# Optimization experiments

Hardware: AMD Instinct MI355X
Metric: run time of the kernel (lower is better)

The kernel has to match this reference:

```python
import jax, jax.numpy as jnp
import numpy as np
import math

D_MODEL = 1024
NUM_HEADS = 16
D_K = D_MODEL // NUM_HEADS
SEQ = 2048
BATCH = 2


def setup_inputs() -> dict:
    key = jax.random.key(0)
    ks = jax.random.split(key, 11)
    s = 1.0 / math.sqrt(D_MODEL)
    return {
        "query": jax.random.normal(ks[0], (SEQ, BATCH, D_MODEL), jnp.float32),
        "key": jax.random.normal(ks[1], (SEQ, BATCH, D_MODEL), jnp.float32),
        "value": jax.random.normal(ks[2], (SEQ, BATCH, D_MODEL), jnp.float32),
        "Wq": jax.random.normal(ks[3], (D_MODEL, D_MODEL), jnp.float32) * s,
        "bq": jnp.zeros((D_MODEL,), jnp.float32),
        "Wk": jax.random.normal(ks[4], (D_MODEL, D_MODEL), jnp.float32) * s,
        "bk": jnp.zeros((D_MODEL,), jnp.float32),
        "Wv": jax.random.normal(ks[5], (D_MODEL, D_MODEL), jnp.float32) * s,
        "bv": jnp.zeros((D_MODEL,), jnp.float32),
        "Wo": jax.random.normal(ks[6], (D_MODEL, D_MODEL), jnp.float32) * s,
        "bo": jnp.zeros((D_MODEL,), jnp.float32),
    }


def _split_heads(x):
    # [S, B, D] -> [S, B, H, d_k]
    S, B, _ = x.shape
    return x.reshape(S, B, NUM_HEADS, D_K)


def reference(query, key, value, Wq, bq, Wk, bk, Wv, bv, Wo, bo):
    # torch Linear: y = x @ W.T + b
    q = _split_heads(query @ Wq.T + bq)   # [S,B,H,dk]
    k = _split_heads(key @ Wk.T + bk)
    v = _split_heads(value @ Wv.T + bv)
    # score[q,k,b,h] = sum_d q[q,b,h,d] k[k,b,h,d]
    score = jnp.einsum('qbhd,kbhd->qkbh', q, k) / math.sqrt(D_K)
    attn = jax.nn.softmax(score, axis=1)  # Softmax(dim=1) == over key axis
    out = jnp.einsum('qkbh,kbhd->qbhd', attn, v)  # [S,B,H,dk]
    S, B = out.shape[0], out.shape[1]
    out = out.reshape(S, B, NUM_HEADS * D_K)
    return out @ Wo.T + bo
```

## Files before the change

### kernel.cpp

```cpp
#include <hip/hip_runtime.h>

typedef unsigned short u16;
typedef short s16x8 __attribute__((ext_vector_type(8)));
typedef short s16x4 __attribute__((ext_vector_type(4)));
typedef float f32x4 __attribute__((ext_vector_type(4)));

#define MFMA_BF16(A,B,C) __builtin_amdgcn_mfma_f32_16x16x32_bf16(A,B,C,0,0,0)

#if defined(__has_builtin)
#if __has_builtin(__builtin_amdgcn_mfma_f32_16x16x16bf16_1k)
#define HAVE_MFMA16 1
#define MFMA16(A,B,C) __builtin_amdgcn_mfma_f32_16x16x16bf16_1k(A,B,C,0,0,0)
#endif
#endif

static constexpr int DMODEL = 1024;
static constexpr int SEQn   = 2048;
static constexpr int BATCH  = 2;
static constexpr int NH     = 16;
static constexpr int DKn    = 64;
static constexpr int ROWST  = BATCH*DMODEL;
static constexpr float QSCALE = 0.18033688011112042f;

__device__ __forceinline__ u16 f2bf(float f) {
    unsigned u = __builtin_bit_cast(unsigned, f);
    u += 0x7FFFu + ((u >> 16) & 1u);
    return (u16)(u >> 16);
}

#if defined(__has_builtin)
#if __has_builtin(__builtin_amdgcn_cvt_pk_bf16_f32)
#define HAVE_PKBF16 1
#endif
#endif
#ifdef HAVE_PKBF16
typedef __bf16 bf16x2 __attribute__((ext_vector_type(2)));
__device__ __forceinline__ unsigned pk2bf(float a, float b) {
    bf16x2 t = __builtin_amdgcn_cvt_pk_bf16_f32(a, b);
    return __builtin_bit_cast(unsigned, t);
}
#else
__device__ __forceinline__ unsigned pk2bf(float a, float b) {
    return (unsigned)f2bf(a) | ((unsigned)f2bf(b) << 16);
}
#endif

__device__ __forceinline__ void gld_lds16(const u16* g, u16* l) {
    __builtin_amdgcn_global_load_lds(
        (const __attribute__((address_space(1))) void*)g,
        (__attribute__((address_space(3))) void*)l,
        16, 0, 0);
}

__global__ void cvt_bf16(const float* __restrict__ q, const float* __restrict__ k,
                         const float* __restrict__ v, const float* __restrict__ wq,
                         const float* __restrict__ wk, const float* __restrict__ wv,
                         const float* __restrict__ wo,
                         u16* __restrict__ qb, u16* __restrict__ kb, u16* __restrict__ vb,
                         u16* __restrict__ wqb, u16* __restrict__ wkb, u16* __restrict__ wvb,
                         u16* __restrict__ wob)
{
    const int z = blockIdx.z;
    const float* S; u16* D; size_t n;
    switch (z) {
        case 0: S = q;  D = qb;  n = 4194304; break;
        case 1: S = k;  D = kb;  n = 4194304; break;
        case 2: S = v;  D = vb;  n = 4194304; break;
        case 3: S = wq; D = wqb; n = 1048576; break;
        case 4: S = wk; D = wkb; n = 1048576; break;
        case 5: S = wv; D = wvb; n = 1048576; break;
        default: S = wo; D = wob; n = 1048576; break;
    }
    const size_t i = ((size_t)blockIdx.x * 256 + threadIdx.x) * 8;
    if (i >= n) return;
    float4 a = *(const float4*)(S + i);
    float4 b = *(const float4*)(S + i + 4);
    uint4 pk;
    pk.x = pk2bf(a.x, a.y); pk.y = pk2bf(a.z, a.w);
    pk.z = pk2bf(b.x, b.y); pk.w = pk2bf(b.z, b.w);
    *(uint4*)(D + i) = pk;
}

template<bool FINAL>
__global__ __launch_bounds__(256, 2)
void gemm_bt(const u16* __restrict__ A0, const u16* __restrict__ A1, const u16* __restrict__ A2,
             const u16* __restrict__ W0, const u16* __restrict__ W1, const u16* __restrict__ W2,
             const float* __restrict__ B0, const float* __restrict__ B1, const float* __restrict__ B2,
             void* __restrict__ O0, void* __restrict__ O1, void* __restrict__ O2)
{
    const u16* A; const u16* W; const float* bias; void* Outv;
    const int z = blockIdx.z;
    if (z == 0)      { A = A0; W = W0; bias = B0; Outv = O0; }
    else if (z == 1) { A = A1; W = W1; bias = B1; Outv = O1; }
    else             { A = A2; W = W2; bias = B2; Outv = O2; }

    __shared__ alignas(16) u16 SH[FINAL ? 128*128 : 129*128];
    u16* As = SH;
    u16* Bs = SH + 128*64;

    const int tid  = threadIdx.x;
    const int wave = tid >> 6, lane = tid & 63;
    const int quad = lane >> 4, col = lane & 15;
    const int wm = wave & 1, wn = wave >> 1;
    const int m0 = blockIdx.y * 128, n0 = blockIdx.x * 128;

    f32x4 acc[4][4];
#pragma unroll
    for (int i = 0; i < 4; ++i)
#pragma unroll
        for (int j = 0; j < 4; ++j) acc[i][j] = f32x4{0.f,0.f,0.f,0.f};

    for (int kt = 0; kt < DMODEL/64; ++kt) {
        if (kt) __syncthreads();
        const int k0 = kt*64;
#pragma unroll
        for (int i = 0; i < 4; ++i) {
            const int chunk = (i*4 + wave)*64 + lane;
            const int row = chunk >> 3;
            const int kk = ((chunk & 7) ^ (row & 7)) * 8;
            gld_lds16(A + (size_t)(m0 + row)*DMODEL + (k0 + kk), &As[(i*4 + wave)*512]);
            gld_lds16(W + (size_t)(n0 + row)*DMODEL + (k0 + kk), &Bs[(i*4 + wave)*512]);
        }
        __syncthreads();
#pragma unroll
        for (int ks = 0; ks < 2; ++ks) {
            s16x8 af[4], bfr[4];
#pragma unroll
            for (int t = 0; t < 4; ++t) {
                const int ra = wm*64 + t*16 + col;
                af[t]  = *(const s16x8*)&As[ra*64 + (((ks*4 + quad) ^ (ra & 7))*8)];
                const int rb = wn*64 + t*16 + col;
                bfr[t] = *(const s16x8*)&Bs[rb*64 + (((ks*4 + quad) ^ (rb & 7))*8)];
            }
#pragma unroll
            for (int i = 0; i < 4; ++i)
#pragma unroll
                for (int j = 0; j < 4; ++j)
                    acc[i][j] = MFMA_BF16(af[i], bfr[j], acc[i][j]);
        }
    }

    float bv[4];
#pragma unroll
    for (int j = 0; j < 4; ++j) bv[j] = bias[n0 + wn*64 + j*16 + col];

    if (FINAL) {
#pragma unroll
        for (int i = 0; i < 4; ++i)
#pragma unroll
            for (int j = 0; j < 4; ++j) {
                const int n = n0 + wn*64 + j*16 + col;
#pragma unroll
                for (int r = 0; r < 4; ++r) {
                    const int m = m0 + wm*64 + i*16 + quad*4 + r;
                    ((float*)Outv)[(size_t)m*DMODEL + n] = acc[i][j][r] + bv[j];
                }
            }
    } else {
        const float osc = (z == 0) ? QSCALE : 1.f;
        const int SST = (z == 2) ? 129 : 128;
        __syncthreads();
#pragma unroll
        for (int i = 0; i < 4; ++i)
#pragma unroll
            for (int j = 0; j < 4; ++j) {
                const int nl = wn*64 + j*16 + col;
#pragma unroll
                for (int r = 0; r < 4; ++r) {
                    const int ml = wm*64 + i*16 + quad*4 + r;
                    SH[ml*SST + nl] = f2bf((acc[i][j][r] + bv[j])*osc);
                }
            }
        __syncthreads();
        u16* Out = (u16*)Outv;
        if (z < 2) {
#pragma unroll
            for (int t = 0; t < 8; ++t) {
                const int c = t*256 + tid;
                const int ml = c >> 4, n8 = (c & 15)*8;
                uint4 x = *(const uint4*)&SH[ml*128 + n8];
                *(uint4*)(Out + (size_t)(m0 + ml)*DMODEL + n0 + n8) = x;
            }
        } else {
            const int s0 = m0 >> 1;
#pragma unroll
            for (int t = 0; t < 8; ++t) {
                const int c = t*256 + tid;
                const int sc = c & 7;
                const int nl = (c >> 3) & 127;
                const int bb = c >> 10;
                u16 e[8];
#pragma unroll
                for (int j = 0; j < 8; ++j)
                    e[j] = SH[((sc*8 + j)*2 + bb)*129 + nl];
                uint4 x; __builtin_memcpy(&x, e, 16);
                const int ng = n0 + nl, hh = ng >> 6, dd = ng & 63;
                *(uint4*)(Out + (((size_t)bb*NH + hh)*DKn + dd)*SEQn + s0 + sc*8) = x;
            }
        }
    }
}

__global__ __launch_bounds__(256, 2)
void attn_fwd(const u16* __restrict__ Q, const u16* __restrict__ K,
              const u16* __restrict__ Vt, u16* __restrict__ O)
{
    __shared__ alignas(16) u16 Ks[128*64];
    __shared__ alignas(16) u16 Vs[64*128];

    const int qt = blockIdx.x, bh = blockIdx.y;
    const int b = bh >> 4, h = bh & 15;
    const int tid = threadIdx.x;
    const int wave = tid >> 6, lane = tid & 63;
    const int quad = lane >> 4, col = lane & 15;

    const u16* Qh = Q + b*DMODEL + h*DKn;
    const u16* Kh = K + b*DMODEL + h*DKn;
    const u16* Vh = Vt + (size_t)bh*DKn*SEQn;

    const int q0 = qt*128 + wave*32;
    s16x8 qf[2][2];
#pragma unroll
    for (int qg = 0; qg < 2; ++qg)
#pragma unroll
        for (int ks = 0; ks < 2; ++ks)
            qf[qg][ks] = *(const s16x8*)(Qh + (size_t)(q0 + qg*16 + col)*ROWST + ks*32 + quad*8);

    f32x4 o[2][4];
    float dsum[2] = {0.f, 0.f};
#pragma unroll
    for (int qg = 0; qg < 2; ++qg)
#pragma unroll
        for (int dt = 0; dt < 4; ++dt) o[qg][dt] = f32x4{0.f,0.f,0.f,0.f};

    for (int kt = 0; kt < SEQn/128; ++kt) {
        __syncthreads();
#pragma unroll
        for (int i = 0; i < 4; ++i) {
            {
                const int chunk = (i*4 + wave)*64 + lane;
                const int row = chunk >> 3;
                const int kk = ((chunk & 7) ^ (row & 7))*8;
                gld_lds16(Kh + (size_t)(kt*128 + row)*ROWST + kk, &Ks[(i*4 + wave)*512]);
            }
            {
                const int chunk = (i*4 + wave)*64 + lane;
                const int d = chunk >> 4;
                const int kk = ((chunk & 15) ^ (d & 15))*8;
                gld_lds16(Vh + (size_t)d*SEQn + kt*128 + kk, &Vs[(i*4 + wave)*512]);
            }
        }
        __syncthreads();

        f32x4 sfr[2][8];
#pragma unroll
        for (int qg = 0; qg < 2; ++qg)
#pragma unroll
            for (int nt = 0; nt < 8; ++nt) sfr[qg][nt] = f32x4{0.f,0.f,0.f,0.f};
#pragma unroll
        for (int ks = 0; ks < 2; ++ks) {
#pragma unroll
            for (int nt = 0; nt < 8; ++nt) {
                const int key = nt*16 + col;
                const s16x8 kf = *(const s16x8*)&Ks[key*64 + (((ks*4 + quad) ^ (key & 7))*8)];
                sfr[0][nt] = MFMA_BF16(kf, qf[0][ks], sfr[0][nt]);
                sfr[1][nt] = MFMA_BF16(kf, qf[1][ks], sfr[1][nt]);
            }
        }

        s16x4 pk[2][8];
#pragma unroll
        for (int qg = 0; qg < 2; ++qg)
#pragma unroll
            for (int nt = 0; nt < 8; ++nt) {
                float p0 = __builtin_amdgcn_exp2f(sfr[qg][nt][0]);
                float p1 = __builtin_amdgcn_exp2f(sfr[qg][nt][1]);
                float p2 = __builtin_amdgcn_exp2f(sfr[qg][nt][2]);
                float p3 = __builtin_amdgcn_exp2f(sfr[qg][nt][3]);
                dsum[qg] += (p0 + p1) + (p2 + p3);
                unsigned w[2] = { pk2bf(p0, p1), pk2bf(p2, p3) };
                __builtin_memcpy(&pk[qg][nt], w, 8);
            }

#ifdef HAVE_MFMA16
#pragma unroll
        for (int c = 0; c < 8; ++c) {
#pragma unroll
            for (int dt = 0; dt < 4; ++dt) {
                const int d = dt*16 + col;
                const s16x4 vfr = *(const s16x4*)&Vs[d*128 + (((c*2 + (quad>>1)) ^ (d & 15))*8) + (quad & 1)*4];
                o[0][dt] = MFMA16(vfr, pk[0][c], o[0][dt]);
                o[1][dt] = MFMA16(vfr, pk[1][c], o[1][dt]);
            }
        }
#else
        const int a0 = (32*(quad & 1) + col)*4;
#pragma unroll
        for (int qg = 0; qg < 2; ++qg) {
#pragma unroll
            for (int ksp = 0; ksp < 4; ++ksp) {
                int pA[2], pB[2];
                __builtin_memcpy(pA, &pk[qg][ksp*2], 8);
                __builtin_memcpy(pB, &pk[qg][ksp*2 + 1], 8);
                int w[4];
#pragma unroll
                for (int hh = 0; hh < 2; ++hh) {
                    const int ad = a0 + hh*64;
                    const int xA0 = __builtin_amdgcn_ds_bpermute(ad, pA[0]);
                    const int xA1 = __builtin_amdgcn_ds_bpermute(ad, pA[1]);
                    const int xB0 = __builtin_amdgcn_ds_bpermute(ad, pB[0]);
                    const int xB1 = __builtin_amdgcn_ds_bpermute(ad, pB[1]);
                    w[hh*2]     = (quad >= 2) ? xB0 : xA0;
                    w[hh*2 + 1] = (quad >= 2) ? xB1 : xA1;
                }
                s16x8 pfr; __builtin_memcpy(&pfr, w, 16);
#pragma unroll
                for (int dt = 0; dt < 4; ++dt) {
                    const int d = dt*16 + col;
                    const s16x8 vfr = *(const s16x8*)&Vs[d*128 + (((ksp*4 + quad) ^ (d & 15))*8)];
                    o[qg][dt] = MFMA_BF16(vfr, pfr, o[qg][dt]);
                }
            }
        }
#endif
    }

    float inv[2];
#pragma unroll
    for (int qg = 0; qg < 2; ++qg) {
        float d = dsum[qg];
        d += __shfl_xor(d, 16, 64);
        d += __shfl_xor(d, 32, 64);
        inv[qg] = 1.f / d;
    }

#pragma unroll
    for (int qg = 0; qg < 2; ++qg) {
        const int srow = q0 + qg*16 + col;
#pragma unroll
        for (int dt = 0; dt < 4; ++dt) {
            uint2 pko;
            pko.x = pk2bf(o[qg][dt][0]*inv[qg], o[qg][dt][1]*inv[qg]);
            pko.y = pk2bf(o[qg][dt][2]*inv[qg], o[qg][dt][3]*inv[qg]);
            *(uint2*)(O + ((size_t)srow*BATCH + b)*DMODEL + h*DKn + dt*16 + quad*4) = pko;
        }
    }
}

extern "C" void kernel_launch(void* const* d_in, const int* in_sizes, int n_in,
                              void* d_out, int out_size, void* d_ws, size_t ws_size,
                              hipStream_t stream)
{
    const float* q  = (const float*)d_in[0];
    const float* k  = (const float*)d_in[1];
    const float* v  = (const float*)d_in[2];
    const float* Wq = (const float*)d_in[3];
    const float* bq = (const float*)d_in[4];
    const float* Wk = (const float*)d_in[5];
    const float* bk = (const float*)d_in[6];
    const float* Wv = (const float*)d_in[7];
    const float* bv = (const float*)d_in[8];
    const float* Wo = (const float*)d_in[9];
    const float* bo = (const float*)d_in[10];
    float* out = (float*)d_out;

    const size_t N = (size_t)SEQn * BATCH * DMODEL;
    const size_t NW = (size_t)DMODEL * DMODEL;
    u16* qb  = (u16*)d_ws;
    u16* kb  = qb + N;
    u16* vb  = kb + N;
    u16* wqb = vb + N;
    u16* wkb = wqb + NW;
    u16* wvb = wkb + NW;
    u16* wob = wvb + NW;
    u16* Qw  = wob + NW;
    u16* Kw  = Qw + N;
    u16* Vtw = Kw + N;
    u16* AO  = qb;

    cvt_bf16<<<dim3(2048, 1, 7), 256, 0, stream>>>(q, k, v, Wq, Wk, Wv, Wo,
                                                   qb, kb, vb, wqb, wkb, wvb, wob);
    gemm_bt<false><<<dim3(8, 32, 3), 256, 0, stream>>>(qb, kb, vb, wqb, wkb, wvb,
                                                       bq, bk, bv, Qw, Kw, Vtw);
    attn_fwd<<<dim3(16, 32), 256, 0, stream>>>(Qw, Kw, Vtw, AO);
    gemm_bt<true><<<dim3(8, 32, 1), 256, 0, stream>>>(AO, AO, AO, wob, wob, wob,
                                                      bo, bo, bo, out, out, out);
}
```

Baseline: 234.6 us.

## Split attention key tiles across waves with cross-wave LDS reduction of outputs

Each block now handles 32 queries instead of 128. The four waves split each 128-key tile among themselves, with 32 keys per wave, instead of each wave owning separate query rows. Partial outputs and denominators are combined across waves through LDS at the end, and the grid grows fourfold with launch bounds raised to 4 blocks per SM. This aims to increase parallelism and occupancy, but every block now reloads the full K and V tiles for only 32 queries, quadrupling K/V traffic, and adds an LDS reduction step.

```diff
diff --git a/kernel.cpp b/kernel.cpp
--- a/kernel.cpp
+++ b/kernel.cpp
@@ -201,12 +201,13 @@
     }
 }
 
-__global__ __launch_bounds__(256, 2)
+__global__ __launch_bounds__(256, 4)
 void attn_fwd(const u16* __restrict__ Q, const u16* __restrict__ K,
               const u16* __restrict__ Vt, u16* __restrict__ O)
 {
-    __shared__ alignas(16) u16 Ks[128*64];
-    __shared__ alignas(16) u16 Vs[64*128];
+    __shared__ alignas(16) u16 SH[16896];
+    u16* Ks = SH;
+    u16* Vs = SH + 128*64;
 
     const int qt = blockIdx.x, bh = blockIdx.y;
     const int b = bh >> 4, h = bh & 15;
@@ -218,33 +219,32 @@
     const u16* Kh = K + b*DMODEL + h*DKn;
     const u16* Vh = Vt + (size_t)bh*DKn*SEQn;
 
-    const int q0 = qt*128 + wave*32;
+    const int q0 = qt*32;
     s16x8 qf[2][2];
 #pragma unroll
-    for (int qg = 0; qg < 2; ++qg)
+    for (int qb = 0; qb < 2; ++qb)
 #pragma unroll
         for (int ks = 0; ks < 2; ++ks)
-            qf[qg][ks] = *(const s16x8*)(Qh + (size_t)(q0 + qg*16 + col)*ROWST + ks*32 + quad*8);
+            qf[qb][ks] = *(const s16x8*)(Qh + (size_t)(q0 + qb*16 + col)*ROWST + ks*32 + quad*8);
 
     f32x4 o[2][4];
     float dsum[2] = {0.f, 0.f};
 #pragma unroll
-    for (int qg = 0; qg < 2; ++qg)
-#pragma unroll
-        for (int dt = 0; dt < 4; ++dt) o[qg][dt] = f32x4{0.f,0.f,0.f,0.f};
+    for (int qb = 0; qb < 2; ++qb)
+#pragma unroll
+        for (int dt = 0; dt < 4; ++dt) o[qb][dt] = f32x4{0.f,0.f,0.f,0.f};
 
     for (int kt = 0; kt < SEQn/128; ++kt) {
-        __syncthreads();
+        if (kt) __syncthreads();
 #pragma unroll
         for (int i = 0; i < 4; ++i) {
+            const int chunk = (i*4 + wave)*64 + lane;
             {
-                const int chunk = (i*4 + wave)*64 + lane;
                 const int row = chunk >> 3;
                 const int kk = ((chunk & 7) ^ (row & 7))*8;
                 gld_lds16(Kh + (size_t)(kt*128 + row)*ROWST + kk, &Ks[(i*4 + wave)*512]);
             }
             {
-                const int chunk = (i*4 + wave)*64 + lane;
                 const int d = chunk >> 4;
                 const int kk = ((chunk & 15) ^ (d & 15))*8;
                 gld_lds16(Vh + (size_t)d*SEQn + kt*128 + kk, &Vs[(i*4 + wave)*512]);
@@ -252,99 +252,113 @@
         }
         __syncthreads();
 
-        f32x4 sfr[2][8];
-#pragma unroll
-        for (int qg = 0; qg < 2; ++qg)
-#pragma unroll
-            for (int nt = 0; nt < 8; ++nt) sfr[qg][nt] = f32x4{0.f,0.f,0.f,0.f};
+        f32x4 sfr[2][2];
+#pragma unroll
+        for (int qb = 0; qb < 2; ++qb)
+#pragma unroll
+            for (int kb = 0; kb < 2; ++kb) sfr[qb][kb] = f32x4{0.f,0.f,0.f,0.f};
 #pragma unroll
         for (int ks = 0; ks < 2; ++ks) {
 #pragma unroll
-            for (int nt = 0; nt < 8; ++nt) {
-                const int key = nt*16 + col;
+            for (int kb = 0; kb < 2; ++kb) {
+                const int key = wave*32 + kb*16 + col;
                 const s16x8 kf = *(const s16x8*)&Ks[key*64 + (((ks*4 + quad) ^ (key & 7))*8)];
-                sfr[0][nt] = MFMA_BF16(kf, qf[0][ks], sfr[0][nt]);
-                sfr[1][nt] = MFMA_BF16(kf, qf[1][ks], sfr[1][nt]);
-            }
-        }
-
-        s16x4 pk[2][8];
-#pragma unroll
-        for (int qg = 0; qg < 2; ++qg)
-#pragma unroll
-            for (int nt = 0; nt < 8; ++nt) {
-                float p0 = __builtin_amdgcn_exp2f(sfr[qg][nt][0]);
-                float p1 = __builtin_amdgcn_exp2f(sfr[qg][nt][1]);
-                float p2 = __builtin_amdgcn_exp2f(sfr[qg][nt][2]);
-                float p3 = __builtin_amdgcn_exp2f(sfr[qg][nt][3]);
-                dsum[qg] += (p0 + p1) + (p2 + p3);
+                sfr[0][kb] = MFMA_BF16(kf, qf[0][ks], sfr[0][kb]);
+                sfr[1][kb] = MFMA_BF16(kf, qf[1][ks], sfr[1][kb]);
+            }
+        }
+
+        s16x4 pk[2][2];
+#pragma unroll
+        for (int qb = 0; qb < 2; ++qb)
+#pragma unroll
+            for (int kb = 0; kb < 2; ++kb) {
+                float p0 = __builtin_amdgcn_exp2f(sfr[qb][kb][0]);
+                float p1 = __builtin_amdgcn_exp2f(sfr[qb][kb][1]);
+                float p2 = __builtin_amdgcn_exp2f(sfr[qb][kb][2]);
+                float p3 = __builtin_amdgcn_exp2f(sfr[qb][kb][3]);
+                dsum[qb] += (p0 + p1) + (p2 + p3);
                 unsigned w[2] = { pk2bf(p0, p1), pk2bf(p2, p3) };
-                __builtin_memcpy(&pk[qg][nt], w, 8);
+                __builtin_memcpy(&pk[qb][kb], w, 8);
             }
 
 #ifdef HAVE_MFMA16
 #pragma unroll
-        for (int c = 0; c < 8; ++c) {
+        for (int kb = 0; kb < 2; ++kb) {
+            const int c = wave*2 + kb;
 #pragma unroll
             for (int dt = 0; dt < 4; ++dt) {
                 const int d = dt*16 + col;
                 const s16x4 vfr = *(const s16x4*)&Vs[d*128 + (((c*2 + (quad>>1)) ^ (d & 15))*8) + (quad & 1)*4];
-                o[0][dt] = MFMA16(vfr, pk[0][c], o[0][dt]);
-                o[1][dt] = MFMA16(vfr, pk[1][c], o[1][dt]);
+                o[0][dt] = MFMA16(vfr, pk[0][kb], o[0][dt]);
+                o[1][dt] = MFMA16(vfr, pk[1][kb], o[1][dt]);
             }
         }
 #else
         const int a0 = (32*(quad & 1) + col)*4;
 #pragma unroll
-        for (int qg = 0; qg < 2; ++qg) {
-#pragma unroll
-            for (int ksp = 0; ksp < 4; ++ksp) {
-                int pA[2], pB[2];
-                __builtin_memcpy(pA, &pk[qg][ksp*2], 8);
-                __builtin_memcpy(pB, &pk[qg][ksp*2 + 1], 8);
-                int w[4];
-#pragma unroll
-                for (int hh = 0; hh < 2; ++hh) {
-                    const int ad = a0 + hh*64;
-                    const int xA0 = __builtin_amdgcn_ds_bpermute(ad, pA[0]);
-                    const int xA1 = __builtin_amdgcn_ds_bpermute(ad, pA[1]);
-                    const int xB0 = __builtin_amdgcn_ds_bpermute(ad, pB[0]);
-                    const int xB1 = __builtin_amdgcn_ds_bpermute(ad, pB[1]);
-                    w[hh*2]     = (quad >= 2) ? xB0 : xA0;
-                    w[hh*2 + 1] = (quad >= 2) ? xB1 : xA1;
-                }
-                s16x8 pfr; __builtin_memcpy(&pfr, w, 16);
-#pragma unroll
-                for (int dt = 0; dt < 4; ++dt) {
-                    const int d = dt*16 + col;
-                    const s16x8 vfr = *(const s16x8*)&Vs[d*128 + (((ksp*4 + quad) ^ (d & 15))*8)];
-                    o[qg][dt] = MFMA_BF16(vfr, pfr, o[qg][dt]);
-                }
-            }
-        }
-#endif
-    }
-
-    float inv[2];
-#pragma unroll
-    for (int qg = 0; qg < 2; ++qg) {
-        float d = dsum[qg];
-        d += __shfl_xor(d, 16, 64);
-        d += __shfl_xor(d, 32, 64);
-        inv[qg] = 1.f / d;
-    }
-
-#pragma unroll
-    for (int qg = 0; qg < 2; ++qg) {
-        const int srow = q0 + qg*16 + col;
+        for (int qb = 0; qb < 2; ++qb) {
+            int pA[2], pB[2];
+            __builtin_memcpy(pA, &pk[qb][0], 8);
+            __builtin_memcpy(pB, &pk[qb][1], 8);
+            int w4[4];
+#pragma unroll
+            for (int hh = 0; hh < 2; ++hh) {
+                const int ad = a0 + hh*64;
+                const int xA0 = __builtin_amdgcn_ds_bpermute(ad, pA[0]);
+                const int xA1 = __builtin_amdgcn_ds_bpermute(ad, pA[1]);
+                const int xB0 = __builtin_amdgcn_ds_bpermute(ad, pB[0]);
+                const int xB1 = __builtin_amdgcn_ds_bpermute(ad, pB[1]);
+                w4[hh*2]     = (quad >= 2) ? xB0 : xA0;
+                w4[hh*2 + 1] = (quad >= 2) ? xB1 : xA1;
+            }
+            s16x8 pfr; __builtin_memcpy(&pfr, w4, 16);
+#pragma unroll
+            for (int dt = 0; dt < 4; ++dt) {
+                const int d = dt*16 + col;
+                const s16x8 vfr = *(const s16x8*)&Vs[d*128 + (((wave*4 + quad) ^ (d & 15))*8)];
+                o[qb][dt] = MFMA_BF16(vfr, pfr, o[qb][dt]);
+            }
+        }
+#endif
+    }
+
+    __syncthreads();
+    float* Ow   = (float*)SH;
+    float* Dsum = Ow + 4*32*65;
+
+#pragma unroll
+    for (int qb = 0; qb < 2; ++qb) {
+        float dw = dsum[qb];
+        dw += __shfl_xor(dw, 16, 64);
+        dw += __shfl_xor(dw, 32, 64);
+        if (quad == 0) Dsum[wave*32 + qb*16 + col] = dw;
+    }
+#pragma unroll
+    for (int qb = 0; qb < 2; ++qb)
 #pragma unroll
         for (int dt = 0; dt < 4; ++dt) {
-            uint2 pko;
-            pko.x = pk2bf(o[qg][dt][0]*inv[qg], o[qg][dt][1]*inv[qg]);
-            pko.y = pk2bf(o[qg][dt][2]*inv[qg], o[qg][dt][3]*inv[qg]);
-            *(uint2*)(O + ((size_t)srow*BATCH + b)*DMODEL + h*DKn + dt*16 + quad*4) = pko;
-        }
-    }
+            const int base = wave*2080 + (qb*16 + col)*65 + dt*16 + quad*4;
+#pragma unroll
+            for (int r = 0; r < 4; ++r) Ow[base + r] = o[qb][dt][r];
+        }
+    __syncthreads();
+
+    const int qq = tid >> 3, d8 = (tid & 7)*8;
+    const float den = Dsum[qq] + Dsum[32 + qq] + Dsum[64 + qq] + Dsum[96 + qq];
+    const float invd = 1.f / den;
+    float s[8];
+#pragma unroll
+    for (int j = 0; j < 8; ++j) {
+        const int idx = qq*65 + d8 + j;
+        s[j] = (Ow[idx] + Ow[idx + 2080]) + (Ow[idx + 4160] + Ow[idx + 6240]);
+    }
+    uint4 pko;
+    pko.x = pk2bf(s[0]*invd, s[1]*invd);
+    pko.y = pk2bf(s[2]*invd, s[3]*invd);
+    pko.z = pk2bf(s[4]*invd, s[5]*invd);
+    pko.w = pk2bf(s[6]*invd, s[7]*invd);
+    *(uint4*)(O + ((size_t)(q0 + qq)*BATCH + b)*DMODEL + h*DKn + d8) = pko;
 }
 
 extern "C" void kernel_launch(void* const* d_in, const int* in_sizes, int n_in,
@@ -382,7 +396,7 @@
                                                    qb, kb, vb, wqb, wkb, wvb, wob);
     gemm_bt<false><<<dim3(8, 32, 3), 256, 0, stream>>>(qb, kb, vb, wqb, wkb, wvb,
                                                        bq, bk, bv, Qw, Kw, Vtw);
-    attn_fwd<<<dim3(16, 32), 256, 0, stream>>>(Qw, Kw, Vtw, AO);
+    attn_fwd<<<dim3(64, 32), 256, 0, stream>>>(Qw, Kw, Vtw, AO);
     gemm_bt<true><<<dim3(8, 32, 1), 256, 0, stream>>>(AO, AO, AO, wob, wob, wob,
                                                       bo, bo, bo, out, out, out);
 }
```

Result: no change. 237.8 us (+1.4%).
